# Kernel tuning notes

Measured on AMD Instinct MI355X. Metric: run time of the kernel, lower is better.

## Reference

```python
import jax, jax.numpy as jnp
import numpy as np

N_NODES = 100000
NEG_SLOPE = 0.01  # torch F.leaky_relu default


def gcn_conv(x, src, dst, norm, W, b):
    # x: [N, Fin]; src/dst: [E+N] (self-loops included); norm: [E+N]
    h = x @ W                                  # [N, Fout] dense transform
    msg = h[src] * norm[:, None]               # gather + edge-wise scale
    out = jax.ops.segment_sum(msg, dst, num_segments=x.shape[0])  # scatter-add
    return out + b


def build_graph(edge_index, n_nodes):
    # Add self-loops and compute symmetric GCN normalization deg^-1/2 * deg^-1/2
    loop = jnp.arange(n_nodes, dtype=edge_index.dtype)
    src = jnp.concatenate([edge_index[0], loop])
    dst = jnp.concatenate([edge_index[1], loop])
    deg = jax.ops.segment_sum(jnp.ones_like(dst, dtype=jnp.float32), dst,
                              num_segments=n_nodes)
    dinv = jnp.where(deg > 0, jax.lax.rsqrt(deg), 0.0)
    norm = dinv[src] * dinv[dst]
    return src, dst, norm


def setup_inputs() -> dict:
    key = jax.random.key(0)
    ks = jax.random.split(key, 8)
    in_c, out_c = 256, 64
    hid = 2 * out_c
    x = jax.random.normal(ks[0], (N_NODES, in_c), dtype=jnp.float32)
    edge_index = jax.random.randint(ks[1], (2, 1600000), 0, N_NODES, dtype=jnp.int64)
    def glorot(k, fan_in, fan_out):
        s = jnp.sqrt(6.0 / (fan_in + fan_out))
        return jax.random.uniform(k, (fan_in, fan_out), jnp.float32, -s, s)
    return {
        "x": x,
        "edge_index": edge_index,
        "W1": glorot(ks[2], in_c, hid),
        "b1": jnp.zeros((hid,), jnp.float32),
        "Wmu": glorot(ks[3], hid, out_c),
        "bmu": jnp.zeros((out_c,), jnp.float32),
        "Wlv": glorot(ks[4], hid, out_c),
        "blv": jnp.zeros((out_c,), jnp.float32),
    }


def reference(x, edge_index, W1, b1, Wmu, bmu, Wlv, blv):
    src, dst, norm = build_graph(edge_index, x.shape[0])
    h = gcn_conv(x, src, dst, norm, W1, b1)
    h = jnp.where(h >= 0, h, NEG_SLOPE * h)  # leaky_relu
    mu = gcn_conv(h, src, dst, norm, Wmu, bmu)
    logvar = gcn_conv(h, src, dst, norm, Wlv, blv)
    return (mu, logvar)
```

## Files before the change

kernel.cpp:

```cpp
#include <hip/hip_runtime.h>

typedef unsigned short bf16_t;
typedef short s16x8 __attribute__((ext_vector_type(8)));
typedef float f32x4 __attribute__((ext_vector_type(4)));


#define NBKT 782
#define BSH  7
#define BMSK 127
#define CAPS 512

__device__ __forceinline__ float bf2f(unsigned short u) {
    unsigned int v = ((unsigned int)u) << 16;
    float f;
    __builtin_memcpy(&f, &v, 4);
    return f;
}
__device__ __forceinline__ unsigned short f2bf(float f) {
    unsigned int x;
    __builtin_memcpy(&x, &f, 4);
    unsigned int r = x + 0x7fffu + ((x >> 16) & 1u);
    return (unsigned short)(r >> 16);
}
__device__ __forceinline__ unsigned pack2(float a, float b) {
    return (unsigned)f2bf(a) | ((unsigned)f2bf(b) << 16);
}
__device__ __forceinline__ float ldf(const void* p, long long i, unsigned f32) {
    return f32 ? ((const float*)p)[i] : bf2f(((const unsigned short*)p)[i]);
}
__device__ __forceinline__ int ldi(const void* p, long long i, unsigned i64) {
    return i64 ? (int)((const long long*)p)[i] : ((const int*)p)[i];
}
__device__ __forceinline__ s16x8 ld8u(const unsigned short* p) {
    return *(const s16x8*)p;
}
__device__ __forceinline__ f32x4 mfma16(s16x8 a, s16x8 b, f32x4 c) {
    return __builtin_amdgcn_mfma_f32_16x16x32_bf16(a, b, c, 0, 0, 0);
}
__device__ __forceinline__ void cvt_hl(const float* p, s16x8& hi, s16x8& lo) {
    const float4 u = *(const float4*)p;
    const float4 w = *(const float4*)(p + 4);
    float v[8] = {u.x, u.y, u.z, u.w, w.x, w.y, w.z, w.w};
#pragma unroll
    for (int j = 0; j < 8; ++j) {
        unsigned short h = f2bf(v[j]);
        hi[j] = (short)h;
        lo[j] = (short)f2bf(v[j] - bf2f(h));
    }
}

__global__ __launch_bounds__(256) void k_detect(const void* x, const void* W1,
                                                const void* ei, unsigned* flags,
                                                int* __restrict__ btail) {
    __shared__ float smx[256];
    __shared__ float smw[256];
    __shared__ int   szc[256];
    int tid = threadIdx.x;
    for (int i = tid; i < NBKT * 8; i += 256) btail[i] = 0;
    const unsigned short* xu = (const unsigned short*)x;
    float mx = 0.f;
    for (int i = tid; i < 4096; i += 256) {
        unsigned short w = xu[i];
        if ((w & 0x7fffu) >= 0x7f80u) mx = 1e30f;
        else { float f = fabsf(bf2f(w)); if (f > mx) mx = f; }
    }
    smx[tid] = mx;
    const unsigned short* wu = (const unsigned short*)W1;
    float mw = 0.f;
    for (int i = tid; i < 4096; i += 256) {
        unsigned short w = wu[i];
        if ((w & 0x7fffu) >= 0x7f80u) mw = 1e30f;
        else { float f = fabsf(bf2f(w)); if (f > mw) mw = f; }
    }
    smw[tid] = mw;
    const int* eu = (const int*)ei;
    int zc = 0;
    for (int i = tid; i < 128; i += 256)
        if ((i & 1) && eu[i] == 0) ++zc;
    szc[tid] = zc;
    __syncthreads();
    for (int off = 128; off > 0; off >>= 1) {
        if (tid < off) {
            if (smx[tid + off] > smx[tid]) smx[tid] = smx[tid + off];
            if (smw[tid + off] > smw[tid]) smw[tid] = smw[tid + off];
            szc[tid] += szc[tid + off];
        }
        __syncthreads();
    }
    if (tid == 0) {
        flags[0] = (smx[0] > 1e4f) ? 1u : 0u;
        flags[1] = (smw[0] > 10.f) ? 1u : 0u;
        flags[2] = (szc[0] >= 56) ? 1u : 0u;
    }
}

__global__ __launch_bounds__(256) void k_bucket(const void* ei, const unsigned* det,
                                                int* __restrict__ btail,
                                                unsigned* __restrict__ bstore,
                                                int E, int N) {
    int e = blockIdx.x * 256 + threadIdx.x;
    if (e >= E) return;
    unsigned i64 = det[2];
    int s = ldi(ei, e, i64);
    int d = ldi(ei, (long long)E + e, i64);
    if ((unsigned)d >= (unsigned)N) return;
    int b = d >> BSH;
    int sub = blockIdx.x & 7;
    int slot = atomicAdd(&btail[sub * NBKT + b], 1);
    if (slot < CAPS) {
        unsigned src = ((unsigned)s < (unsigned)N) ? (unsigned)s : (unsigned)d;
        bstore[((long long)(b * 8 + sub)) * CAPS + slot] =
            ((unsigned)(d & BMSK) << 24) | src;
    }
}

__global__ __launch_bounds__(256) void k_bhist(const int* __restrict__ btail,
                                               const unsigned* __restrict__ bstore,
                                               int* __restrict__ cnt,
                                               float* __restrict__ dinv, int N) {
    __shared__ int lh[128];
    __shared__ int ln[8];
    const int b = blockIdx.x;
    const int tid = threadIdx.x;
    if (tid < 128) lh[tid] = 0;
    if (tid < 8) {
        int t = btail[tid * NBKT + b];
        ln[tid] = t < CAPS ? t : CAPS;
    }
    __syncthreads();
#pragma unroll 1
    for (int s = 0; s < 8; ++s) {
        int n = ln[s];
        const unsigned* base = &bstore[((long long)(b * 8 + s)) * CAPS];
        for (int i = tid; i < n; i += 256)
            atomicAdd(&lh[base[i] >> 24], 1);
    }
    __syncthreads();
    int node = b * 128 + tid;
    if (tid < 128 && node < N) {
        cnt[node] = lh[tid];
        dinv[node] = rsqrtf((float)lh[tid] + 1.0f);
    }
}

__global__ __launch_bounds__(256) void k_scan_blk(const int* __restrict__ cnt,
                                                  int* __restrict__ pos,
                                                  int* __restrict__ bsum, int N) {
    __shared__ int sh[256];
    const int tid = threadIdx.x;
    const int base = blockIdx.x * 1024 + tid * 4;
    int v[4];
#pragma unroll
    for (int j = 0; j < 4; ++j) v[j] = (base + j < N) ? cnt[base + j] : 0;
    int s = v[0] + v[1] + v[2] + v[3];
    sh[tid] = s;
    __syncthreads();
    for (int off = 1; off < 256; off <<= 1) {
        int t = (tid >= off) ? sh[tid - off] : 0;
        __syncthreads();
        sh[tid] += t;
        __syncthreads();
    }
    int run = sh[tid] - s;
#pragma unroll
    for (int j = 0; j < 4; ++j) {
        if (base + j < N) pos[base + j] = run;
        run += v[j];
    }
    if (tid == 255) bsum[blockIdx.x] = sh[255];
}

__global__ __launch_bounds__(256) void k_scan_add(int* __restrict__ pos,
                                                  const int* __restrict__ bsum, int N) {
    __shared__ int sadd;
    if (threadIdx.x == 0) {
        int a = 0;
        for (int i = 0; i < blockIdx.x; ++i) a += bsum[i];
        sadd = a;
    }
    __syncthreads();
    int add = sadd;
    int base = blockIdx.x * 1024;
    for (int i = threadIdx.x; i < 1024; i += 256)
        if (base + i < N) pos[base + i] += add;
}

__global__ __launch_bounds__(256) void k_emit(const int* __restrict__ btail,
                                              const unsigned* __restrict__ bstore,
                                              const int* __restrict__ pos,
                                              int* __restrict__ srt, int N) {
    __shared__ int lstart[128];
    __shared__ int loff[128];
    __shared__ int ln[8];
    __shared__ int stage[4096];
    const int b = blockIdx.x;
    const int tid = threadIdx.x;
    const int base0 = pos[b * 128];
    if (tid < 128) {
        int node = b * 128 + tid;
        lstart[tid] = (node < N) ? (pos[node] - base0) : 0;
        loff[tid] = 0;
    }
    if (tid < 8) {
        int t = btail[tid * NBKT + b];
        ln[tid] = t < CAPS ? t : CAPS;
    }
    __syncthreads();
#pragma unroll 1
    for (int s = 0; s < 8; ++s) {
        int n = ln[s];
        const unsigned* bp = &bstore[((long long)(b * 8 + s)) * CAPS];
        for (int i = tid; i < n; i += 256) {
            unsigned rec = bp[i];
            int dl = rec >> 24;
            int slot = atomicAdd(&loff[dl], 1);
            stage[lstart[dl] + slot] = (int)(rec & 0xffffffu);
        }
    }
    __syncthreads();
    int total = ln[0] + ln[1] + ln[2] + ln[3] + ln[4] + ln[5] + ln[6] + ln[7];
    for (int i = tid; i < total; i += 256)
        srt[base0 + i] = stage[i];
}

__global__ __launch_bounds__(256) void k_wsplit(const void* W1, const void* Wmu,
                                                const void* Wlv, const unsigned* det,
                                                unsigned short* __restrict__ bt1h,
                                                unsigned short* __restrict__ bt1l,
                                                unsigned short* __restrict__ bt2h,
                                                unsigned short* __restrict__ bt2l) {
    int idx = blockIdx.x * 256 + threadIdx.x;
    unsigned wf = det[1];
    if (idx < 256 * 128) {
        int k = idx >> 7, n = idx & 127;
        float w = ldf(W1, idx, wf);
        unsigned short h = f2bf(w);
        bt1h[(long long)n * 256 + k] = h;
        bt1l[(long long)n * 256 + k] = f2bf(w - bf2f(h));
    } else if (idx < 256 * 128 + 128 * 128) {
        int j = idx - 256 * 128;
        int k = j >> 7, n = j & 127;
        float w = (n < 64) ? ldf(Wmu, (long long)k * 64 + n, wf)
                           : ldf(Wlv, (long long)k * 64 + (n - 64), wf);
        unsigned short h = f2bf(w);
        bt2h[(long long)n * 128 + k] = h;
        bt2l[(long long)n * 128 + k] = f2bf(w - bf2f(h));
    }
}

__global__ __launch_bounds__(256, 2) void k_gemm1p(
    const void* __restrict__ x, const unsigned* __restrict__ det,
    const unsigned short* __restrict__ bth,
    const unsigned short* __restrict__ btl,
    const float* __restrict__ dinv,
    unsigned* __restrict__ Cp, int N) {
    const int lane = threadIdx.x & 63;
    const int wid  = threadIdx.x >> 6;
    const int wr = wid >> 1, wc = wid & 1;
    const int l15 = lane & 15, lg = lane >> 4;
    const long long r0 = (long long)blockIdx.x * 64 + wr * 32;
    long long ar[2];
#pragma unroll
    for (int m = 0; m < 2; ++m) {
        long long r = r0 + m * 16 + l15;
        ar[m] = (r < N) ? r : (N - 1);
    }
    int bn[4];
#pragma unroll
    for (int n = 0; n < 4; ++n) bn[n] = wc * 64 + n * 16 + l15;

    f32x4 acc[2][4] = {};
    if (!det[0]) {
        const unsigned short* xp = (const unsigned short*)x;
        const unsigned short* aP[2];
#pragma unroll
        for (int m = 0; m < 2; ++m) aP[m] = xp + ar[m] * 256 + lg * 8;
        const unsigned short* bHp[4];
        const unsigned short* bLp[4];
#pragma unroll
        for (int n = 0; n < 4; ++n) {
            bHp[n] = bth + (long long)bn[n] * 256 + lg * 8;
            bLp[n] = btl + (long long)bn[n] * 256 + lg * 8;
        }
        s16x8 aS[8][2], bhS[2][4], blS[2][4];
#pragma unroll
        for (int s = 0; s < 2; ++s)
#pragma unroll
            for (int m = 0; m < 2; ++m) aS[s][m] = ld8u(aP[m] + s * 32);
#pragma unroll
        for (int n = 0; n < 4; ++n) {
            bhS[0][n] = ld8u(bHp[n]);
            blS[0][n] = ld8u(bLp[n]);
        }
#pragma unroll
        for (int st = 0; st < 8; ++st) {
            if (st < 7) {
                const int nb = (st + 1) & 1;
#pragma unroll
                for (int n = 0; n < 4; ++n) {
                    bhS[nb][n] = ld8u(bHp[n] + (st + 1) * 32);
                    blS[nb][n] = ld8u(bLp[n] + (st + 1) * 32);
                }
            }
            if (st < 6) {
#pragma unroll
                for (int m = 0; m < 2; ++m)
                    aS[st + 2][m] = ld8u(aP[m] + (st + 2) * 32);
            }
            const int cb = st & 1;
#pragma unroll
            for (int m = 0; m < 2; ++m)
#pragma unroll
                for (int n = 0; n < 4; ++n) {
                    acc[m][n] = mfma16(aS[st][m], bhS[cb][n], acc[m][n]);
                    acc[m][n] = mfma16(aS[st][m], blS[cb][n], acc[m][n]);
                }
        }
    } else {
        const float* xp = (const float*)x;
#pragma unroll 2
        for (int k0 = 0; k0 < 256; k0 += 32) {
            const int kb = k0 + lg * 8;
            s16x8 ah[2], al[2], bh[4], bl[4];
#pragma unroll
            for (int m = 0; m < 2; ++m) cvt_hl(xp + ar[m] * 256 + kb, ah[m], al[m]);
#pragma unroll
            for (int n = 0; n < 4; ++n) {
                bh[n] = ld8u(bth + (long long)bn[n] * 256 + kb);
                bl[n] = ld8u(btl + (long long)bn[n] * 256 + kb);
            }
#pragma unroll
            for (int m = 0; m < 2; ++m)
#pragma unroll
                for (int n = 0; n < 4; ++n) {
                    acc[m][n] = mfma16(ah[m], bh[n], acc[m][n]);
                    acc[m][n] = mfma16(ah[m], bl[n], acc[m][n]);
                    acc[m][n] = mfma16(al[m], bh[n], acc[m][n]);
                }
        }
    }
#pragma unroll
    for (int m = 0; m < 2; ++m)
#pragma unroll
        for (int n = 0; n < 4; ++n) {
            const int col = wc * 64 + n * 16 + l15;
#pragma unroll
            for (int r = 0; r < 4; ++r) {
                long long row = r0 + m * 16 + lg * 4 + r;
                float v = acc[m][n][r] * dinv[(row < N) ? row : (N - 1)];
                float p = __shfl_xor(v, 1);
                if (!(lane & 1) && row < N)
                    Cp[row * 64 + (col >> 1)] = pack2(v, p);
            }
        }
}

__global__ __launch_bounds__(256, 2) void k_gemm2p(
    const unsigned short* __restrict__ hap,
    const unsigned short* __restrict__ bth,
    const unsigned short* __restrict__ btl,
    const void* bmu, const void* blv, const unsigned* __restrict__ det,
    float* __restrict__ outMu, float* __restrict__ outLv, int N) {
    const int lane = threadIdx.x & 63;
    const int wid  = threadIdx.x >> 6;
    const int wr = wid >> 1, wc = wid & 1;
    const int l15 = lane & 15, lg = lane >> 4;
    const long long r0 = (long long)blockIdx.x * 64 + wr * 32;
    long long ar[2];
#pragma unroll
    for (int m = 0; m < 2; ++m) {
        long long r = r0 + m * 16 + l15;
        ar[m] = (r < N) ? r : (N - 1);
    }
    int bn[4];
#pragma unroll
    for (int n = 0; n < 4; ++n) bn[n] = wc * 64 + n * 16 + l15;

    const unsigned short* aP[2];
#pragma unroll
    for (int m = 0; m < 2; ++m) aP[m] = hap + ar[m] * 128 + lg * 8;
    const unsigned short* bHp[4];
    const unsigned short* bLp[4];
#pragma unroll
    for (int n = 0; n < 4; ++n) {
        bHp[n] = bth + (long long)bn[n] * 128 + lg * 8;
        bLp[n] = btl + (long long)bn[n] * 128 + lg * 8;
    }
    f32x4 acc[2][4] = {};
    s16x8 aS[4][2], bhS[2][4], blS[2][4];
#pragma unroll
    for (int s = 0; s < 2; ++s)
#pragma unroll
        for (int m = 0; m < 2; ++m) aS[s][m] = ld8u(aP[m] + s * 32);
#pragma unroll
    for (int n = 0; n < 4; ++n) {
        bhS[0][n] = ld8u(bHp[n]);
        blS[0][n] = ld8u(bLp[n]);
    }
#pragma unroll
    for (int st = 0; st < 4; ++st) {
        if (st < 3) {
            const int nb = (st + 1) & 1;
#pragma unroll
            for (int n = 0; n < 4; ++n) {
                bhS[nb][n] = ld8u(bHp[n] + (st + 1) * 32);
                blS[nb][n] = ld8u(bLp[n] + (st + 1) * 32);
            }
        }
        if (st < 2) {
#pragma unroll
            for (int m = 0; m < 2; ++m)
                aS[st + 2][m] = ld8u(aP[m] + (st + 2) * 32);
        }
        const int cb = st & 1;
#pragma unroll
        for (int m = 0; m < 2; ++m)
#pragma unroll
            for (int n = 0; n < 4; ++n) {
                acc[m][n] = mfma16(aS[st][m], bhS[cb][n], acc[m][n]);
                acc[m][n] = mfma16(aS[st][m], blS[cb][n], acc[m][n]);
            }
    }
    __syncthreads();
    const unsigned wf = det[1];
#pragma unroll
    for (int m = 0; m < 2; ++m)
#pragma unroll
        for (int n = 0; n < 4; ++n) {
            const int col = wc * 64 + n * 16 + l15;
            const float bias = (col < 64) ? ldf(bmu, col, wf)
                                          : ldf(blv, col - 64, wf);
#pragma unroll
            for (int r = 0; r < 4; ++r) {
                long long row = r0 + m * 16 + lg * 4 + r;
                if (row < N) {
                    float v = acc[m][n][r] + bias;
                    if (col < 64) outMu[row * 64 + col] = v;
                    else          outLv[row * 64 + (col - 64)] = v;
                }
            }
        }
}

__global__ __launch_bounds__(256) void k_gather(const uint2* __restrict__ hp2,
                                                const int* __restrict__ srt,
                                                const int* __restrict__ cnt,
                                                const int* __restrict__ pos,
                                                const float* __restrict__ dinv,
                                                const void* bias, const unsigned* det,
                                                int leaky, int prescaleOut,
                                                uint2* __restrict__ outp2, int N) {
    int node = blockIdx.x * 8 + (threadIdx.x >> 5);
    if (node >= N) return;
    int lane5 = threadIdx.x & 31;
    int beg = pos[node];
    int end = beg + cnt[node];
    float dd = dinv[node];
    uint2 hv = hp2[(long long)node * 32 + lane5];
    float a0 = bf2f((unsigned short)(hv.x & 0xffffu));
    float a1 = bf2f((unsigned short)(hv.x >> 16));
    float a2 = bf2f((unsigned short)(hv.y & 0xffffu));
    float a3 = bf2f((unsigned short)(hv.y >> 16));
    for (int q = beg; q < end; q += 8) {
        int s[8];
        uint2 v[8];
#pragma unroll
        for (int j = 0; j < 8; ++j) {
            int qq = q + j;
            s[j] = srt[(qq < end) ? qq : beg];
        }
#pragma unroll
        for (int j = 0; j < 8; ++j)
            v[j] = hp2[(long long)s[j] * 32 + lane5];
#pragma unroll
        for (int j = 0; j < 8; ++j) {
            bool on = (q + j) < end;
            a0 += on ? bf2f((unsigned short)(v[j].x & 0xffffu)) : 0.f;
            a1 += on ? bf2f((unsigned short)(v[j].x >> 16)) : 0.f;
            a2 += on ? bf2f((unsigned short)(v[j].y & 0xffffu)) : 0.f;
            a3 += on ? bf2f((unsigned short)(v[j].y >> 16)) : 0.f;
        }
    }
    a0 *= dd; a1 *= dd; a2 *= dd; a3 *= dd;
    if (bias) {
        a0 += ldf(bias, 4 * lane5 + 0, det[1]);
        a1 += ldf(bias, 4 * lane5 + 1, det[1]);
        a2 += ldf(bias, 4 * lane5 + 2, det[1]);
        a3 += ldf(bias, 4 * lane5 + 3, det[1]);
    }
    if (leaky) {
        a0 = (a0 >= 0.f) ? a0 : 0.01f * a0;
        a1 = (a1 >= 0.f) ? a1 : 0.01f * a1;
        a2 = (a2 >= 0.f) ? a2 : 0.01f * a2;
        a3 = (a3 >= 0.f) ? a3 : 0.01f * a3;
    }
    if (prescaleOut) { a0 *= dd; a1 *= dd; a2 *= dd; a3 *= dd; }
    uint2 o;
    o.x = pack2(a0, a1);
    o.y = pack2(a2, a3);
    outp2[(long long)node * 32 + lane5] = o;
}

__global__ void k_sentinel(float* out, long long lvOff) {
    if (threadIdx.x == 0 && blockIdx.x == 0) {
        out[0] = 9.99e5f;
        out[lvOff] = 9.98e5f;
    }
}

extern "C" void kernel_launch(void* const* d_in, const int* in_sizes, int n_in,
                              void* d_out, int out_size, void* d_ws, size_t ws_size,
                              hipStream_t stream) {
    (void)out_size;
    const int N = 100000, E = 1600000;
    bool ok = (n_in == 8) && in_sizes[0] == 25600000 && in_sizes[1] == 3200000 &&
              in_sizes[2] == 32768 && in_sizes[3] == 128 &&
              in_sizes[4] == 8192 && in_sizes[5] == 64 &&
              in_sizes[6] == 8192 && in_sizes[7] == 64 &&
              ws_size >= (size_t)21 * 1024 * 1024;
    if (!ok) {
        k_sentinel<<<1, 64, 0, stream>>>((float*)d_out, (long long)N * 64);
        return;
    }
    const void* x   = d_in[0];
    const void* ei  = d_in[1];
    const void* W1  = d_in[2];
    const void* b1  = d_in[3];
    const void* Wmu = d_in[4];
    const void* bmu = d_in[5];
    const void* Wlv = d_in[6];
    const void* blv = d_in[7];

    char* w = (char*)d_ws;
    auto carve = [&](size_t bytes) {
        char* p = w;
        w += (bytes + 255) & ~(size_t)255;
        return p;
    };
    unsigned* flags = (unsigned*)carve(64);
    int*    cnt  = (int*)carve((size_t)N * 4);
    int*    pos  = (int*)carve((size_t)N * 4);
    float*  dinv = (float*)carve((size_t)N * 4);
    int*    bsum = (int*)carve(4096);
    int*    srt  = (int*)carve((size_t)E * 4);
    unsigned short* bt1h = (unsigned short*)carve(128 * 256 * 2);
    unsigned short* bt1l = (unsigned short*)carve(128 * 256 * 2);
    unsigned short* bt2h = (unsigned short*)carve(128 * 128 * 2);
    unsigned short* bt2l = (unsigned short*)carve(128 * 128 * 2);
    int*      btail  = (int*)carve((size_t)NBKT * 8 * 4);
    unsigned* bstore = (unsigned*)carve((size_t)NBKT * 8 * CAPS * 4);

    float* M = (float*)d_out;
    float* L = M + (size_t)N * 64;
    unsigned* Mp = (unsigned*)M;
    unsigned* Lp = (unsigned*)L;

    const int nb = (N + 1023) / 1024;
    const int ggrid = N / 8;
    const int gb64 = (N + 63) / 64;

    k_detect<<<1, 256, 0, stream>>>(x, W1, ei, flags, btail);
    k_wsplit<<<(256 * 128 + 128 * 128 + 255) / 256, 256, 0, stream>>>(
        W1, Wmu, Wlv, flags, bt1h, bt1l, bt2h, bt2l);

    k_bucket<<<(E + 255) / 256, 256, 0, stream>>>(ei, flags, btail, bstore, E, N);
    k_bhist<<<NBKT, 256, 0, stream>>>(btail, bstore, cnt, dinv, N);
    k_scan_blk<<<nb, 256, 0, stream>>>(cnt, pos, bsum, N);
    k_scan_add<<<nb, 256, 0, stream>>>(pos, bsum, N);
    k_emit<<<NBKT, 256, 0, stream>>>(btail, bstore, pos, srt, N);

    k_gemm1p<<<gb64, 256, 0, stream>>>(x, flags, bt1h, bt1l, dinv, Mp, N);
    k_gather<<<ggrid, 256, 0, stream>>>((const uint2*)Mp, srt, cnt, pos, dinv,
                                        b1, flags, 1, 1, (uint2*)Lp, N);
    k_gather<<<ggrid, 256, 0, stream>>>((const uint2*)Lp, srt, cnt, pos, dinv,
                                        nullptr, flags, 0, 0, (uint2*)Mp, N);
    k_gemm2p<<<gb64, 256, 0, stream>>>((const unsigned short*)Mp, bt2h, bt2l,
                                       bmu, blv, flags, M, L, N);
}
```

Measured before the change: 527.3 us.

## Widen gather to 16-byte loads per lane and simplify GEMM load pipelines

The gather kernel now gives each node 16 lanes, each loading a uint4 (8 bf16 values), instead of 32 lanes loading uint2. This halves the number of load instructions per neighbor row and packs 16 nodes into each block. Both GEMM kernels drop their hand-written double-buffered register prefetch in favor of a plain unrolled k-loop, and hoist the dinv and bias loads ahead of the main loop. The intent is fewer, wider memory transactions in the gather-bound phase, at the risk of lower memory-level parallelism per node and less explicit latency hiding in the GEMMs.

```diff
diff --git a/kernel.cpp b/kernel.cpp
--- a/kernel.cpp
+++ b/kernel.cpp
@@ -269,51 +269,35 @@
 #pragma unroll
     for (int n = 0; n < 4; ++n) bn[n] = wc * 64 + n * 16 + l15;
 
+    float dv[2][4];
+#pragma unroll
+    for (int m = 0; m < 2; ++m)
+#pragma unroll
+        for (int r = 0; r < 4; ++r) {
+            long long row = r0 + m * 16 + lg * 4 + r;
+            dv[m][r] = dinv[(row < N) ? row : (N - 1)];
+        }
+
     f32x4 acc[2][4] = {};
     if (!det[0]) {
         const unsigned short* xp = (const unsigned short*)x;
-        const unsigned short* aP[2];
-#pragma unroll
-        for (int m = 0; m < 2; ++m) aP[m] = xp + ar[m] * 256 + lg * 8;
-        const unsigned short* bHp[4];
-        const unsigned short* bLp[4];
-#pragma unroll
-        for (int n = 0; n < 4; ++n) {
-            bHp[n] = bth + (long long)bn[n] * 256 + lg * 8;
-            bLp[n] = btl + (long long)bn[n] * 256 + lg * 8;
-        }
-        s16x8 aS[8][2], bhS[2][4], blS[2][4];
-#pragma unroll
-        for (int s = 0; s < 2; ++s)
-#pragma unroll
-            for (int m = 0; m < 2; ++m) aS[s][m] = ld8u(aP[m] + s * 32);
-#pragma unroll
-        for (int n = 0; n < 4; ++n) {
-            bhS[0][n] = ld8u(bHp[n]);
-            blS[0][n] = ld8u(bLp[n]);
-        }
-#pragma unroll
-        for (int st = 0; st < 8; ++st) {
-            if (st < 7) {
-                const int nb = (st + 1) & 1;
+#pragma unroll
+        for (int k0 = 0; k0 < 256; k0 += 32) {
+            const int kb = k0 + lg * 8;
+            s16x8 a[2], bh[4], bl[4];
+#pragma unroll
+            for (int m = 0; m < 2; ++m) a[m] = ld8u(xp + ar[m] * 256 + kb);
+#pragma unroll
+            for (int n = 0; n < 4; ++n) {
+                bh[n] = ld8u(bth + (long long)bn[n] * 256 + kb);
+                bl[n] = ld8u(btl + (long long)bn[n] * 256 + kb);
+            }
+#pragma unroll
+            for (int m = 0; m < 2; ++m)
 #pragma unroll
                 for (int n = 0; n < 4; ++n) {
-                    bhS[nb][n] = ld8u(bHp[n] + (st + 1) * 32);
-                    blS[nb][n] = ld8u(bLp[n] + (st + 1) * 32);
-                }
-            }
-            if (st < 6) {
-#pragma unroll
-                for (int m = 0; m < 2; ++m)
-                    aS[st + 2][m] = ld8u(aP[m] + (st + 2) * 32);
-            }
-            const int cb = st & 1;
-#pragma unroll
-            for (int m = 0; m < 2; ++m)
-#pragma unroll
-                for (int n = 0; n < 4; ++n) {
-                    acc[m][n] = mfma16(aS[st][m], bhS[cb][n], acc[m][n]);
-                    acc[m][n] = mfma16(aS[st][m], blS[cb][n], acc[m][n]);
+                    acc[m][n] = mfma16(a[m], bh[n], acc[m][n]);
+                    acc[m][n] = mfma16(a[m], bl[n], acc[m][n]);
                 }
         }
     } else {
@@ -347,7 +331,7 @@
 #pragma unroll
             for (int r = 0; r < 4; ++r) {
                 long long row = r0 + m * 16 + lg * 4 + r;
-                float v = acc[m][n][r] * dinv[(row < N) ? row : (N - 1)];
+                float v = acc[m][n][r] * dv[m][r];
                 float p = __shfl_xor(v, 1);
                 if (!(lane & 1) && row < N)
                     Cp[row * 64 + (col >> 1)] = pack2(v, p);
@@ -376,65 +360,45 @@
 #pragma unroll
     for (int n = 0; n < 4; ++n) bn[n] = wc * 64 + n * 16 + l15;
 
-    const unsigned short* aP[2];
-#pragma unroll
-    for (int m = 0; m < 2; ++m) aP[m] = hap + ar[m] * 128 + lg * 8;
-    const unsigned short* bHp[4];
-    const unsigned short* bLp[4];
+    const unsigned wf = det[1];
+    float bs[4];
 #pragma unroll
     for (int n = 0; n < 4; ++n) {
-        bHp[n] = bth + (long long)bn[n] * 128 + lg * 8;
-        bLp[n] = btl + (long long)bn[n] * 128 + lg * 8;
-    }
+        const int col = wc * 64 + n * 16 + l15;
+        bs[n] = (col < 64) ? ldf(bmu, col, wf) : ldf(blv, col - 64, wf);
+    }
+
     f32x4 acc[2][4] = {};
-    s16x8 aS[4][2], bhS[2][4], blS[2][4];
-#pragma unroll
-    for (int s = 0; s < 2; ++s)
-#pragma unroll
-        for (int m = 0; m < 2; ++m) aS[s][m] = ld8u(aP[m] + s * 32);
-#pragma unroll
-    for (int n = 0; n < 4; ++n) {
-        bhS[0][n] = ld8u(bHp[n]);
-        blS[0][n] = ld8u(bLp[n]);
-    }
-#pragma unroll
-    for (int st = 0; st < 4; ++st) {
-        if (st < 3) {
-            const int nb = (st + 1) & 1;
+#pragma unroll
+    for (int k0 = 0; k0 < 128; k0 += 32) {
+        const int kb = k0 + lg * 8;
+        s16x8 a[2], bh[4], bl[4];
+#pragma unroll
+        for (int m = 0; m < 2; ++m) a[m] = ld8u(hap + ar[m] * 128 + kb);
+#pragma unroll
+        for (int n = 0; n < 4; ++n) {
+            bh[n] = ld8u(bth + (long long)bn[n] * 128 + kb);
+            bl[n] = ld8u(btl + (long long)bn[n] * 128 + kb);
+        }
+#pragma unroll
+        for (int m = 0; m < 2; ++m)
 #pragma unroll
             for (int n = 0; n < 4; ++n) {
-                bhS[nb][n] = ld8u(bHp[n] + (st + 1) * 32);
-                blS[nb][n] = ld8u(bLp[n] + (st + 1) * 32);
+                acc[m][n] = mfma16(a[m], bh[n], acc[m][n]);
+                acc[m][n] = mfma16(a[m], bl[n], acc[m][n]);
             }
-        }
-        if (st < 2) {
-#pragma unroll
-            for (int m = 0; m < 2; ++m)
-                aS[st + 2][m] = ld8u(aP[m] + (st + 2) * 32);
-        }
-        const int cb = st & 1;
-#pragma unroll
-        for (int m = 0; m < 2; ++m)
-#pragma unroll
-            for (int n = 0; n < 4; ++n) {
-                acc[m][n] = mfma16(aS[st][m], bhS[cb][n], acc[m][n]);
-                acc[m][n] = mfma16(aS[st][m], blS[cb][n], acc[m][n]);
-            }
-    }
-    __syncthreads();
-    const unsigned wf = det[1];
+    }
+    __syncthreads();
 #pragma unroll
     for (int m = 0; m < 2; ++m)
 #pragma unroll
         for (int n = 0; n < 4; ++n) {
             const int col = wc * 64 + n * 16 + l15;
-            const float bias = (col < 64) ? ldf(bmu, col, wf)
-                                          : ldf(blv, col - 64, wf);
 #pragma unroll
             for (int r = 0; r < 4; ++r) {
                 long long row = r0 + m * 16 + lg * 4 + r;
                 if (row < N) {
-                    float v = acc[m][n][r] + bias;
+                    float v = acc[m][n][r] + bs[n];
                     if (col < 64) outMu[row * 64 + col] = v;
                     else          outLv[row * 64 + (col - 64)] = v;
                 }
@@ -442,28 +406,33 @@
         }
 }
 
-__global__ __launch_bounds__(256) void k_gather(const uint2* __restrict__ hp2,
+__global__ __launch_bounds__(256) void k_gather(const uint4* __restrict__ hp4,
                                                 const int* __restrict__ srt,
                                                 const int* __restrict__ cnt,
                                                 const int* __restrict__ pos,
                                                 const float* __restrict__ dinv,
                                                 const void* bias, const unsigned* det,
                                                 int leaky, int prescaleOut,
-                                                uint2* __restrict__ outp2, int N) {
-    int node = blockIdx.x * 8 + (threadIdx.x >> 5);
+                                                uint4* __restrict__ outp4, int N) {
+    int node = blockIdx.x * 16 + (threadIdx.x >> 4);
     if (node >= N) return;
-    int lane5 = threadIdx.x & 31;
+    int lane4 = threadIdx.x & 15;
     int beg = pos[node];
     int end = beg + cnt[node];
     float dd = dinv[node];
-    uint2 hv = hp2[(long long)node * 32 + lane5];
-    float a0 = bf2f((unsigned short)(hv.x & 0xffffu));
-    float a1 = bf2f((unsigned short)(hv.x >> 16));
-    float a2 = bf2f((unsigned short)(hv.y & 0xffffu));
-    float a3 = bf2f((unsigned short)(hv.y >> 16));
+    uint4 hv = hp4[(long long)node * 16 + lane4];
+    float a[8];
+    a[0] = bf2f((unsigned short)(hv.x & 0xffffu));
+    a[1] = bf2f((unsigned short)(hv.x >> 16));
+    a[2] = bf2f((unsigned short)(hv.y & 0xffffu));
+    a[3] = bf2f((unsigned short)(hv.y >> 16));
+    a[4] = bf2f((unsigned short)(hv.z & 0xffffu));
+    a[5] = bf2f((unsigned short)(hv.z >> 16));
+    a[6] = bf2f((unsigned short)(hv.w & 0xffffu));
+    a[7] = bf2f((unsigned short)(hv.w >> 16));
     for (int q = beg; q < end; q += 8) {
         int s[8];
-        uint2 v[8];
+        uint4 v[8];
 #pragma unroll
         for (int j = 0; j < 8; ++j) {
             int qq = q + j;
@@ -471,34 +440,40 @@
         }
 #pragma unroll
         for (int j = 0; j < 8; ++j)
-            v[j] = hp2[(long long)s[j] * 32 + lane5];
+            v[j] = hp4[(long long)s[j] * 16 + lane4];
 #pragma unroll
         for (int j = 0; j < 8; ++j) {
             bool on = (q + j) < end;
-            a0 += on ? bf2f((unsigned short)(v[j].x & 0xffffu)) : 0.f;
-            a1 += on ? bf2f((unsigned short)(v[j].x >> 16)) : 0.f;
-            a2 += on ? bf2f((unsigned short)(v[j].y & 0xffffu)) : 0.f;
-            a3 += on ? bf2f((unsigned short)(v[j].y >> 16)) : 0.f;
-        }
-    }
-    a0 *= dd; a1 *= dd; a2 *= dd; a3 *= dd;
+            a[0] += on ? bf2f((unsigned short)(v[j].x & 0xffffu)) : 0.f;
+            a[1] += on ? bf2f((unsigned short)(v[j].x >> 16)) : 0.f;
+            a[2] += on ? bf2f((unsigned short)(v[j].y & 0xffffu)) : 0.f;
+            a[3] += on ? bf2f((unsigned short)(v[j].y >> 16)) : 0.f;
+            a[4] += on ? bf2f((unsigned short)(v[j].z & 0xffffu)) : 0.f;
+            a[5] += on ? bf2f((unsigned short)(v[j].z >> 16)) : 0.f;
+            a[6] += on ? bf2f((unsigned short)(v[j].w & 0xffffu)) : 0.f;
+            a[7] += on ? bf2f((unsigned short)(v[j].w >> 16)) : 0.f;
+        }
+    }
+#pragma unroll
+    for (int t = 0; t < 8; ++t) a[t] *= dd;
     if (bias) {
-        a0 += ldf(bias, 4 * lane5 + 0, det[1]);
-        a1 += ldf(bias, 4 * lane5 + 1, det[1]);
-        a2 += ldf(bias, 4 * lane5 + 2, det[1]);
-        a3 += ldf(bias, 4 * lane5 + 3, det[1]);
+#pragma unroll
+        for (int t = 0; t < 8; ++t) a[t] += ldf(bias, 8 * lane4 + t, det[1]);
     }
     if (leaky) {
-        a0 = (a0 >= 0.f) ? a0 : 0.01f * a0;
-        a1 = (a1 >= 0.f) ? a1 : 0.01f * a1;
-        a2 = (a2 >= 0.f) ? a2 : 0.01f * a2;
-        a3 = (a3 >= 0.f) ? a3 : 0.01f * a3;
-    }
-    if (prescaleOut) { a0 *= dd; a1 *= dd; a2 *= dd; a3 *= dd; }
-    uint2 o;
-    o.x = pack2(a0, a1);
-    o.y = pack2(a2, a3);
-    outp2[(long long)node * 32 + lane5] = o;
+#pragma unroll
+        for (int t = 0; t < 8; ++t) a[t] = (a[t] >= 0.f) ? a[t] : 0.01f * a[t];
+    }
+    if (prescaleOut) {
+#pragma unroll
+        for (int t = 0; t < 8; ++t) a[t] *= dd;
+    }
+    uint4 o;
+    o.x = pack2(a[0], a[1]);
+    o.y = pack2(a[2], a[3]);
+    o.z = pack2(a[4], a[5]);
+    o.w = pack2(a[6], a[7]);
+    outp4[(long long)node * 16 + lane4] = o;
 }
 
 __global__ void k_sentinel(float* out, long long lvOff) {
@@ -556,7 +531,7 @@
     unsigned* Lp = (unsigned*)L;
 
     const int nb = (N + 1023) / 1024;
-    const int ggrid = N / 8;
+    const int ggrid = N / 16;
     const int gb64 = (N + 63) / 64;
 
     k_detect<<<1, 256, 0, stream>>>(x, W1, ei, flags, btail);
@@ -570,10 +545,10 @@
     k_emit<<<NBKT, 256, 0, stream>>>(btail, bstore, pos, srt, N);
 
     k_gemm1p<<<gb64, 256, 0, stream>>>(x, flags, bt1h, bt1l, dinv, Mp, N);
-    k_gather<<<ggrid, 256, 0, stream>>>((const uint2*)Mp, srt, cnt, pos, dinv,
-                                        b1, flags, 1, 1, (uint2*)Lp, N);
-    k_gather<<<ggrid, 256, 0, stream>>>((const uint2*)Lp, srt, cnt, pos, dinv,
-                                        nullptr, flags, 0, 0, (uint2*)Mp, N);
+    k_gather<<<ggrid, 256, 0, stream>>>((const uint4*)Mp, srt, cnt, pos, dinv,
+                                        b1, flags, 1, 1, (uint4*)Lp, N);
+    k_gather<<<ggrid, 256, 0, stream>>>((const uint4*)Lp, srt, cnt, pos, dinv,
+                                        nullptr, flags, 0, 0, (uint4*)Mp, N);
     k_gemm2p<<<gb64, 256, 0, stream>>>((const unsigned short*)Mp, bt2h, bt2l,
                                        bmu, blv, flags, M, L, N);
 }
```

Measured after the change: 538.8 us. +2.2%, slower.
